# Kernel optimization log

Measured on AMD Instinct MI355X. Metric: run time of the kernel, lower is better.

Reference implementation:

```python
import jax, jax.numpy as jnp
import numpy as np

B, L, V = 2048, 200, 100000
EMB_DIM = 32      # emb_session_dim / emb_loc_dim (hardcoded 32 in __init__)
TIME_DIM = 128    # config['model']['timeemb']
LOC_DIM = 32
COND = TIME_DIM + LOC_DIM  # 160
NUM_STEPS = 50
MASK_TIME = 48    # pe[pos == 48] = 0 in the 2-D branch


def _time_embedding(pos, d_model):
    # sinusoidal embedding, interleaved sin/cos exactly as the torch code
    div = 1.0 / jnp.power(10000.0, jnp.arange(0, d_model, 2, dtype=jnp.float32) / d_model)
    ang = pos[..., None].astype(jnp.float32) * div           # [..., d_model//2]
    pe = jnp.zeros(pos.shape + (d_model,), jnp.float32)
    pe = pe.at[..., 0::2].set(jnp.sin(ang)).at[..., 1::2].set(jnp.cos(ang))
    return pe


def setup_inputs() -> dict:
    key = jax.random.key(0)
    ks = jax.random.split(key, 12)
    tp = jax.random.randint(ks[0], (B,), 0, 48, dtype=jnp.int32)
    loc = jax.random.randint(ks[1], (B,), 1, V + 1)            # 1-based loc ids
    emb = jax.random.normal(ks[2], (B, EMB_DIM), jnp.float32)
    s = jax.random.randint(ks[3], (B, L), 1, V + 1)
    tt = jax.random.randint(ks[4], (B, L), 0, 49)              # 48 == padding slot
    ST_traj = jnp.stack([s, tt], axis=-1)                      # [B, L, 2]
    loc_emb_all = jax.random.normal(ks[5], (V, LOC_DIM), jnp.float32) * 0.1
    noise = jax.random.normal(ks[6], (B, EMB_DIM), jnp.float32)
    t = jax.random.randint(ks[7], (B,), 0, NUM_STEPS)
    sc = COND ** -0.5
    w1 = jax.random.normal(ks[8], (COND, COND), jnp.float32) * sc
    w2 = jax.random.normal(ks[9], (COND, COND), jnp.float32) * sc
    b2 = jnp.zeros((COND,), jnp.float32)
    wc = jax.random.normal(ks[10], (COND,), jnp.float32) * sc
    beta = np.linspace(0.0001 ** 0.5, 0.5 ** 0.5, NUM_STEPS) ** 2  # 'quad' schedule
    alpha_hat = jnp.asarray(np.cumprod(1.0 - beta), jnp.float32)
    return {"tp": tp, "loc": loc, "emb": emb, "ST_traj": ST_traj,
            "loc_emb_all": loc_emb_all, "noise": noise, "t": t,
            "w1": w1, "w2": w2, "b2": b2, "wc": wc, "alpha_hat": alpha_hat}


def reference(tp, loc, emb, ST_traj, loc_emb_all, noise, t, w1, w2, b2, wc, alpha_hat):
    # --- diffusion noising (calc_loss prelude) ---
    a = alpha_hat[t][:, None]                                   # [B, 1]
    noisy = jnp.sqrt(a) * emb + jnp.sqrt(1.0 - a) * noise       # [B, EMB_DIM]

    # --- get_ST_info: sinusoid + single fused gather (replaces per-element index_select loop) ---
    te = _time_embedding(tp, TIME_DIM)                          # [B, TIME_DIM] (1-D branch: no mask)
    le = loc_emb_all[loc - 1]                                   # [B, LOC_DIM]
    side = jnp.concatenate([te, le], axis=-1)                   # [B, COND]
    ST_info = jnp.broadcast_to(side[:, :, None], (B, COND, EMB_DIM))

    # --- get_user_info: trajectory embed + soft_attn ---
    s = ST_traj[..., 0]
    ts = ST_traj[..., 1]
    te2 = _time_embedding(ts, TIME_DIM)                         # [B, L, TIME_DIM]
    te2 = jnp.where((ts == MASK_TIME)[..., None], 0.0, te2)     # pe[pos == 48] = 0
    le2 = loc_emb_all[s - 1]                                    # [B, L, LOC_DIM] fused gather
    ue = jnp.concatenate([le2, te2], axis=-1)                   # [B, L, COND]
    mean_e = jnp.mean(ue, axis=1, keepdims=True)                # [B, 1, COND]
    attn = jax.nn.sigmoid(mean_e @ w1.T + ue @ w2.T + b2)       # [B, L, COND]
    score = attn @ wc                                           # [B, L]  (weight_c)
    uemb = jnp.einsum('bl,bld->bd', score, ue)                  # [B, COND]
    user_info = jnp.broadcast_to(uemb[:, :, None], (B, COND, EMB_DIM))

    # pack: [B, 2*COND + 1, EMB_DIM]
    return jnp.concatenate([ST_info, user_info, noisy[:, None, :]], axis=1)
```

## Files before the change

kernel.cpp:

```cpp
#include <hip/hip_runtime.h>
#include <hip/hip_bf16.h>

#define LSEQ   200
#define LPAD   208
#define EMB    32
#define TDIM   128
#define COND   160
#define ROWS   321
#define MASK_T 48
#define LL_LDB 80

typedef __attribute__((ext_vector_type(8))) short          short8;
typedef __attribute__((ext_vector_type(4))) float          f32x4;

__device__ __forceinline__ float bf2f(unsigned short u) {
    union { unsigned int i; float f; } v; v.i = ((unsigned int)u) << 16; return v.f;
}
__device__ __forceinline__ float asf(unsigned int u) {
    union { unsigned int i; float f; } v; v.i = u; return v.f;
}
__device__ __forceinline__ unsigned int f2bf(float f) {
    union { float f; unsigned int i; } v; v.f = f;
    unsigned int x = v.i;
    return ((x + 0x7fffu + ((x >> 16) & 1u)) >> 16);
}
__device__ __forceinline__ unsigned int pack2(float lo, float hi) {
    return f2bf(lo) | (f2bf(hi) << 16);
}

template<int CTRL>
__device__ __forceinline__ float dpp_add(float v) {
    const int x = __builtin_amdgcn_update_dpp(0, __float_as_int(v), CTRL, 0xf, 0xf, true);
    return v + __int_as_float(x);
}
__device__ __forceinline__ float red16(float v) {
    v = dpp_add<0x128>(v);
    v = dpp_add<0x124>(v);
    v = dpp_add<0x122>(v);
    v = dpp_add<0x121>(v);
    return v;
}

__global__ void prep(const float* __restrict__ w1, const float* __restrict__ w2,
                     unsigned short* __restrict__ te_tab, float* __restrict__ T1t,
                     unsigned short* __restrict__ te_t, unsigned short* __restrict__ T2w3,
                     unsigned short* __restrict__ w2b) {
    __shared__ float te128[TDIM];
    const int t = blockIdx.x, tid = threadIdx.x;
    if (tid < 64) {
        const float dv = __expf(-0.14391156f * (float)tid);
        const float a  = (float)t * dv;
        const float s  = __sinf(a), c = __cosf(a);
        te128[2 * tid] = s; te128[2 * tid + 1] = c;
        ((unsigned int*)te_tab)[t * 64 + tid] = pack2(s, c);
    }
    __syncthreads();
    if (tid < COND) {
        float s1 = 0.0f, s2 = 0.0f;
        const float* w1r = w1 + tid * COND + EMB;
        const float* w2r = w2 + tid * COND + EMB;
        #pragma unroll 8
        for (int j = 0; j < TDIM; ++j) {
            s1 = fmaf(te128[j], w1r[j], s1);
            s2 = fmaf(te128[j], w2r[j], s2);
        }
        if (t == MASK_T) { s1 = 0.0f; s2 = 0.0f; }
        T1t[tid * 52 + t] = s1;
        const int tile = tid >> 4, lcc = tid & 15;
        T2w3[t * 256 + lcc * 16 + tile] = (unsigned short)f2bf(s2);
    }
    if (tid < TDIM) te_t[tid * 52 + t] = (unsigned short)f2bf(te128[tid]);
    if (t == 0 && tid < COND) {
        const float* src = w2 + (size_t)tid * COND;
        unsigned int* dst = (unsigned int*)(w2b + tid * 32);
        #pragma unroll
        for (int j = 0; j < 16; ++j)
            dst[j] = pack2(src[2 * j], src[2 * j + 1]);
    }
}

__global__ __launch_bounds__(256) __attribute__((amdgpu_waves_per_eu(4, 8)))
void fused4(const int*   __restrict__ tp,
            const int*   __restrict__ loc,
            const float* __restrict__ emb,
            const int*   __restrict__ st,
            const float* __restrict__ loc_emb,
            const float* __restrict__ noise,
            const int*   __restrict__ tstep,
            const float* __restrict__ w1,
            const unsigned short* __restrict__ w2b,
            const unsigned short* __restrict__ te_tab,
            const float* __restrict__ T1t,
            const unsigned short* __restrict__ te_t,
            const unsigned short* __restrict__ T2w3,
            const float* __restrict__ b2,
            const float* __restrict__ wc,
            const float* __restrict__ alpha_hat,
            float* __restrict__ out)
{
    __shared__ __attribute__((aligned(16))) unsigned char LL[LPAD * LL_LDB];
    __shared__ float scoreW[LSEQ];
    __shared__ float su[320];
    __shared__ float m1W[COND];
    __shared__ __attribute__((aligned(16))) float mupart[4][EMB];
    __shared__ __attribute__((aligned(16))) float cntsb[52];
    __shared__ __attribute__((aligned(4)))  unsigned char ttr[LPAD];

    const int tid  = threadIdx.x;
    const int w    = tid >> 6, lane = tid & 63;
    const int b    = blockIdx.x;
    const int lc   = lane & 15, lg = lane >> 4;
    const int rsub = lane >> 3, csub = lane & 7;
    const int2* st2 = (const int2*)st;
    float* outb = out + (size_t)b * (ROWS * EMB);

    short8 bf[10]; float wcv[10];
    #pragma unroll
    for (int T = 0; T < 10; ++T) {
        const int c = T * 16 + lc;
        bf[T]  = *(const short8*)(w2b + c * 32 + lg * 8);
        wcv[T] = wc[c];
    }

    if (w == 0) {
        if (lane < 32) {
            const ushort4 tv = *(const ushort4*)(te_tab + tp[b] * TDIM + lane * 4);
            f32x4 s4 = { bf2f(tv.x), bf2f(tv.y), bf2f(tv.z), bf2f(tv.w) };
            *(f32x4*)(su + lane * 4) = s4;
        } else if (lane < 40) {
            *(f32x4*)(su + 128 + (lane - 32) * 4) =
                *(const f32x4*)(loc_emb + (size_t)(loc[b] - 1) * EMB + (lane - 32) * 4);
        } else if (lane < 48) {
            const int e4 = lane - 40;
            const float a  = alpha_hat[tstep[b]];
            const float sa = sqrtf(a), sn = sqrtf(1.0f - a);
            const f32x4 ev = *(const f32x4*)(emb + (size_t)b * EMB + e4 * 4);
            const f32x4 nv = *(const f32x4*)(noise + (size_t)b * EMB + e4 * 4);
            f32x4 r = { sa*ev[0]+sn*nv[0], sa*ev[1]+sn*nv[1],
                        sa*ev[2]+sn*nv[2], sa*ev[3]+sn*nv[3] };
            *(f32x4*)(outb + 320 * EMB + e4 * 4) = r;
        }
    } else if (w == 1) {
        if (lane < 52) cntsb[lane] = 0.0f;
        if (lane >= 52 && lane < 60) {
            const int r = 200 + lane - 52;
            uint4 z = make_uint4(0, 0, 0, 0);
            *(uint4*)(LL + r * LL_LDB)      = z;
            *(uint4*)(LL + r * LL_LDB + 16) = z;
            *(uint4*)(LL + r * LL_LDB + 32) = z;
            *(uint4*)(LL + r * LL_LDB + 48) = z;
            ttr[r] = 0;
        }
    }
    __syncthreads();

    int tA = MASK_T;
    if (lane < 50) {
        const int r = w * 50 + lane;
        const int2 sv = st2[(size_t)b * LSEQ + r];
        ttr[r] = (unsigned char)sv.y;
        tA = sv.y;
        if (sv.y != MASK_T) atomicAdd(&cntsb[sv.y], 1.0f);
    }

    f32x4 macc = {0.f, 0.f, 0.f, 0.f};
    #pragma unroll
    for (int i = 0; i < 7; ++i) {
        const int rr = i * 8 + rsub;
        if (rr < 50) {
            const int row = w * 50 + rr;
            const int s0 = st2[(size_t)b * LSEQ + row].x - 1;
            const f32x4 v = *(const f32x4*)(loc_emb + (size_t)s0 * EMB + csub * 4);
            macc += v;
            uint2 pv = make_uint2(pack2(v[0], v[1]), pack2(v[2], v[3]));
            *(uint2*)(LL + row * LL_LDB + csub * 8) = pv;
        }
    }
    #pragma unroll
    for (int sh = 8; sh < 64; sh <<= 1) {
        macc[0] += __shfl_xor(macc[0], sh);
        macc[1] += __shfl_xor(macc[1], sh);
        macc[2] += __shfl_xor(macc[2], sh);
        macc[3] += __shfl_xor(macc[3], sh);
    }
    if (rsub == 0) *(f32x4*)(&mupart[w][csub * 4]) = macc;
    __syncthreads();

    if (tid < COND) {
        const int c = tid;
        f32x4 mm[8];
        #pragma unroll
        for (int j = 0; j < 8; ++j)
            mm[j] = ((const f32x4*)mupart[0])[j] + ((const f32x4*)mupart[1])[j]
                  + ((const f32x4*)mupart[2])[j] + ((const f32x4*)mupart[3])[j];
        f32x4 d = {0.f, 0.f, 0.f, 0.f};
        const f32x4* w1r = (const f32x4*)(w1 + (size_t)c * COND);
        #pragma unroll
        for (int j = 0; j < 8; ++j) d += mm[j] * w1r[j];
        const f32x4* t1r = (const f32x4*)(T1t + c * 52);
        #pragma unroll
        for (int q = 0; q < 13; ++q)
            d += ((const f32x4*)cntsb)[q] * t1r[q];
        m1W[c] = b2[c] + (d[0] + d[1] + d[2] + d[3]) * 0.005f;
    }
    __syncthreads();

    if (w == 1 && lane < 52) cntsb[lane] = 0.0f;

    float m1v[10];
    #pragma unroll
    for (int T = 0; T < 10; ++T) m1v[T] = m1W[T * 16 + lc];

    const int ms   = (w == 0) ? 0 : 3 * w + 1;
    const int mcnt = (w == 0) ? 4 : 3;
    for (int mi = 0; mi < mcnt; ++mi) {
        const int m = ms + mi;
        const short8 av = *(const short8*)(LL + (m * 16 + lc) * LL_LDB + lg * 16);
        const uchar4 tq = *(const uchar4*)(ttr + m * 16 + lg * 4);
        float s4[4] = {0.f, 0.f, 0.f, 0.f};

        #pragma unroll
        for (int g = 0; g < 2; ++g) {
            f32x4 acc[5];
            #pragma unroll
            for (int T5 = 0; T5 < 5; ++T5) {
                f32x4 z = {0.f, 0.f, 0.f, 0.f};
                acc[T5] = __builtin_amdgcn_mfma_f32_16x16x32_bf16(av, bf[g * 5 + T5], z, 0, 0, 0);
            }
            #pragma unroll
            for (int r = 0; r < 4; ++r) {
                const int t = (r == 0) ? tq.x : (r == 1) ? tq.y : (r == 2) ? tq.z : tq.w;
                const unsigned short* t2p = T2w3 + t * 256 + lc * 16 + g * 5;
                const ushort4 qa = *(const ushort4*)(t2p);
                const unsigned short q4 = t2p[4];
                #pragma unroll
                for (int T5 = 0; T5 < 5; ++T5) {
                    const int T = g * 5 + T5;
                    const unsigned short t2u =
                        (T5 == 0) ? qa.x : (T5 == 1) ? qa.y :
                        (T5 == 2) ? qa.z : (T5 == 3) ? qa.w : q4;
                    const float x = acc[T5][r] + m1v[T] + bf2f(t2u);
                    s4[r] = fmaf(wcv[T], __builtin_amdgcn_rcpf(1.0f + __expf(-x)), s4[r]);
                }
            }
        }
        f32x4 srow;
        srow[0] = red16(s4[0]); srow[1] = red16(s4[1]);
        srow[2] = red16(s4[2]); srow[3] = red16(s4[3]);
        if (lc == 0) {
            #pragma unroll
            for (int r = 0; r < 4; ++r) {
                const int row = m * 16 + lg * 4 + r;
                if (row < LSEQ) scoreW[row] = srow[r];
            }
        }
    }
    __syncthreads();

    if (lane < 50) {
        const float sc = scoreW[w * 50 + lane];
        if (tA != MASK_T) atomicAdd(&cntsb[tA], sc);
    }
    f32x4 uacc = {0.f, 0.f, 0.f, 0.f};
    #pragma unroll
    for (int i = 0; i < 7; ++i) {
        const int rr = i * 8 + rsub;
        if (rr < 50) {
            const int row = w * 50 + rr;
            const float sc = scoreW[row];
            const uint2 pv = *(const uint2*)(LL + row * LL_LDB + csub * 8);
            uacc[0] = fmaf(sc, asf(pv.x << 16), uacc[0]);
            uacc[1] = fmaf(sc, asf(pv.x & 0xffff0000u), uacc[1]);
            uacc[2] = fmaf(sc, asf(pv.y << 16), uacc[2]);
            uacc[3] = fmaf(sc, asf(pv.y & 0xffff0000u), uacc[3]);
        }
    }
    #pragma unroll
    for (int sh = 8; sh < 64; sh <<= 1) {
        uacc[0] += __shfl_xor(uacc[0], sh);
        uacc[1] += __shfl_xor(uacc[1], sh);
        uacc[2] += __shfl_xor(uacc[2], sh);
        uacc[3] += __shfl_xor(uacc[3], sh);
    }
    if (rsub == 0) *(f32x4*)(&mupart[w][csub * 4]) = uacc;
    __syncthreads();

    if (tid < TDIM) {
        const int j = tid;
        const unsigned short* ter = te_t + j * 52;
        float s = 0.0f;
        #pragma unroll
        for (int q = 0; q < 13; ++q) {
            const f32x4 sq = ((const f32x4*)cntsb)[q];
            const ushort4 tv = *(const ushort4*)(ter + q * 4);
            s = fmaf(sq[0], bf2f(tv.x), s);
            s = fmaf(sq[1], bf2f(tv.y), s);
            s = fmaf(sq[2], bf2f(tv.z), s);
            s = fmaf(sq[3], bf2f(tv.w), s);
        }
        su[192 + j] = s;
    } else if (tid < TDIM + 32) {
        const int col = tid - TDIM;
        su[160 + col] = mupart[0][col] + mupart[1][col]
                      + mupart[2][col] + mupart[3][col];
    }
    __syncthreads();

    #pragma unroll
    for (int k = 0; k < 10; ++k) {
        const int idx = tid + k * 256;
        const int row = idx >> 3;
        const float v = su[row];
        f32x4 vv = {v, v, v, v};
        *(f32x4*)(outb + row * EMB + (idx & 7) * 4) = vv;
    }
}

extern "C" void kernel_launch(void* const* d_in, const int* in_sizes, int n_in,
                              void* d_out, int out_size, void* d_ws, size_t ws_size,
                              hipStream_t stream) {
    const int*   tp        = (const int*)  d_in[0];
    const int*   loc       = (const int*)  d_in[1];
    const float* emb       = (const float*)d_in[2];
    const int*   st        = (const int*)  d_in[3];
    const float* loc_emb   = (const float*)d_in[4];
    const float* noise     = (const float*)d_in[5];
    const int*   tstep     = (const int*)  d_in[6];
    const float* w1        = (const float*)d_in[7];
    const float* w2        = (const float*)d_in[8];
    const float* b2        = (const float*)d_in[9];
    const float* wc        = (const float*)d_in[10];
    const float* alpha_hat = (const float*)d_in[11];
    float* out = (float*)d_out;

    char* ws = (char*)d_ws;
    float*          T1t    = (float*)ws;
    unsigned short* te_tab = (unsigned short*)(ws + 33280);
    unsigned short* te_t   = (unsigned short*)(ws + 45824);
    unsigned short* T2w3   = (unsigned short*)(ws + 59136);
    unsigned short* w2b    = (unsigned short*)(ws + 84224);

    prep<<<49, 256, 0, stream>>>(w1, w2, te_tab, T1t, te_t, T2w3, w2b);

    const int nb = in_sizes[0];
    fused4<<<nb, 256, 0, stream>>>(tp, loc, emb, st, loc_emb, noise, tstep,
                                   w1, w2b, te_tab, T1t, te_t, T2w3,
                                   b2, wc, alpha_hat, out);
}
```

Before: 71.71 us.

## Split attention score work across waves by output-column tiles instead of rows

Each wave now owns a slice of the 10 output column tiles (3,3,2,2) and loops over all 13 row blocks, instead of owning a range of rows with all 10 column tiles. Per-wave register use for the w2 B-fragments, m1 and wc values drops from 10 tiles to at most 3. The T2 table is re-laid out so each wave's slots are contiguous. Partial scores are combined with LDS atomicAdd into a zero-initialised scoreW. The trade-off is that every wave now reloads all A fragments and adds LDS atomics, in exchange for lower register pressure and a more even load across waves.

```diff
diff --git a/kernel.cpp b/kernel.cpp
--- a/kernel.cpp
+++ b/kernel.cpp
@@ -43,7 +43,7 @@
 
 __global__ void prep(const float* __restrict__ w1, const float* __restrict__ w2,
                      unsigned short* __restrict__ te_tab, float* __restrict__ T1t,
-                     unsigned short* __restrict__ te_t, unsigned short* __restrict__ T2w3,
+                     unsigned short* __restrict__ te_t, unsigned short* __restrict__ T2w4,
                      unsigned short* __restrict__ w2b) {
     __shared__ float te128[TDIM];
     const int t = blockIdx.x, tid = threadIdx.x;
@@ -67,7 +67,9 @@
         if (t == MASK_T) { s1 = 0.0f; s2 = 0.0f; }
         T1t[tid * 52 + t] = s1;
         const int tile = tid >> 4, lcc = tid & 15;
-        T2w3[t * 256 + lcc * 16 + tile] = (unsigned short)f2bf(s2);
+        const int wg   = (tile < 3) ? 0 : (tile < 6) ? 1 : (tile < 8) ? 2 : 3;
+        const int slot = tile - ((wg == 0) ? 0 : (wg == 1) ? 3 : (wg == 2) ? 6 : 8);
+        T2w4[t * 256 + lcc * 16 + wg * 4 + slot] = (unsigned short)f2bf(s2);
     }
     if (tid < TDIM) te_t[tid * 52 + t] = (unsigned short)f2bf(te128[tid]);
     if (t == 0 && tid < COND) {
@@ -92,7 +94,7 @@
             const unsigned short* __restrict__ te_tab,
             const float* __restrict__ T1t,
             const unsigned short* __restrict__ te_t,
-            const unsigned short* __restrict__ T2w3,
+            const unsigned short* __restrict__ T2w4,
             const float* __restrict__ b2,
             const float* __restrict__ wc,
             const float* __restrict__ alpha_hat,
@@ -113,14 +115,6 @@
     const int rsub = lane >> 3, csub = lane & 7;
     const int2* st2 = (const int2*)st;
     float* outb = out + (size_t)b * (ROWS * EMB);
-
-    short8 bf[10]; float wcv[10];
-    #pragma unroll
-    for (int T = 0; T < 10; ++T) {
-        const int c = T * 16 + lc;
-        bf[T]  = *(const short8*)(w2b + c * 32 + lg * 8);
-        wcv[T] = wc[c];
-    }
 
     if (w == 0) {
         if (lane < 32) {
@@ -142,6 +136,10 @@
         }
     } else if (w == 1) {
         if (lane < 52) cntsb[lane] = 0.0f;
+        if (lane < 50) {
+            f32x4 z = {0.f, 0.f, 0.f, 0.f};
+            *(f32x4*)(scoreW + lane * 4) = z;
+        }
         if (lane >= 52 && lane < 60) {
             const int r = 200 + lane - 52;
             uint4 z = make_uint4(0, 0, 0, 0);
@@ -207,51 +205,48 @@
 
     if (w == 1 && lane < 52) cntsb[lane] = 0.0f;
 
-    float m1v[10];
-    #pragma unroll
-    for (int T = 0; T < 10; ++T) m1v[T] = m1W[T * 16 + lc];
-
-    const int ms   = (w == 0) ? 0 : 3 * w + 1;
-    const int mcnt = (w == 0) ? 4 : 3;
-    for (int mi = 0; mi < mcnt; ++mi) {
-        const int m = ms + mi;
+    const int  t0  = (w < 2) ? 3 * w : 6 + 2 * (w - 2);
+    const bool tn3 = (w < 2);
+    short8 bf0, bf1, bf2v = short8{0,0,0,0,0,0,0,0};
+    float m10, m11, m12 = 0.0f, wc0, wc1, wc2 = 0.0f;
+    {
+        const int c0 = t0 * 16 + lc, c1 = (t0 + 1) * 16 + lc;
+        bf0 = *(const short8*)(w2b + c0 * 32 + lg * 8);
+        bf1 = *(const short8*)(w2b + c1 * 32 + lg * 8);
+        m10 = m1W[c0]; wc0 = wc[c0];
+        m11 = m1W[c1]; wc1 = wc[c1];
+        if (tn3) {
+            const int c2 = (t0 + 2) * 16 + lc;
+            bf2v = *(const short8*)(w2b + c2 * 32 + lg * 8);
+            m12 = m1W[c2]; wc2 = wc[c2];
+        }
+    }
+
+    for (int m = 0; m < 13; ++m) {
         const short8 av = *(const short8*)(LL + (m * 16 + lc) * LL_LDB + lg * 16);
         const uchar4 tq = *(const uchar4*)(ttr + m * 16 + lg * 4);
-        float s4[4] = {0.f, 0.f, 0.f, 0.f};
-
-        #pragma unroll
-        for (int g = 0; g < 2; ++g) {
-            f32x4 acc[5];
-            #pragma unroll
-            for (int T5 = 0; T5 < 5; ++T5) {
-                f32x4 z = {0.f, 0.f, 0.f, 0.f};
-                acc[T5] = __builtin_amdgcn_mfma_f32_16x16x32_bf16(av, bf[g * 5 + T5], z, 0, 0, 0);
-            }
-            #pragma unroll
-            for (int r = 0; r < 4; ++r) {
-                const int t = (r == 0) ? tq.x : (r == 1) ? tq.y : (r == 2) ? tq.z : tq.w;
-                const unsigned short* t2p = T2w3 + t * 256 + lc * 16 + g * 5;
-                const ushort4 qa = *(const ushort4*)(t2p);
-                const unsigned short q4 = t2p[4];
-                #pragma unroll
-                for (int T5 = 0; T5 < 5; ++T5) {
-                    const int T = g * 5 + T5;
-                    const unsigned short t2u =
-                        (T5 == 0) ? qa.x : (T5 == 1) ? qa.y :
-                        (T5 == 2) ? qa.z : (T5 == 3) ? qa.w : q4;
-                    const float x = acc[T5][r] + m1v[T] + bf2f(t2u);
-                    s4[r] = fmaf(wcv[T], __builtin_amdgcn_rcpf(1.0f + __expf(-x)), s4[r]);
-                }
-            }
-        }
+        f32x4 z = {0.f, 0.f, 0.f, 0.f};
+        f32x4 a0 = __builtin_amdgcn_mfma_f32_16x16x32_bf16(av, bf0, z, 0, 0, 0);
+        f32x4 a1 = __builtin_amdgcn_mfma_f32_16x16x32_bf16(av, bf1, z, 0, 0, 0);
+        f32x4 a2 = z;
+        if (tn3) a2 = __builtin_amdgcn_mfma_f32_16x16x32_bf16(av, bf2v, z, 0, 0, 0);
+
         f32x4 srow;
-        srow[0] = red16(s4[0]); srow[1] = red16(s4[1]);
-        srow[2] = red16(s4[2]); srow[3] = red16(s4[3]);
+        #pragma unroll
+        for (int r = 0; r < 4; ++r) {
+            const int t = (r == 0) ? tq.x : (r == 1) ? tq.y : (r == 2) ? tq.z : tq.w;
+            const ushort4 q = *(const ushort4*)(T2w4 + t * 256 + lc * 16 + w * 4);
+            float s = wc0 * __builtin_amdgcn_rcpf(1.0f + __expf(-(a0[r] + m10 + bf2f(q.x))))
+                    + wc1 * __builtin_amdgcn_rcpf(1.0f + __expf(-(a1[r] + m11 + bf2f(q.y))));
+            if (tn3)
+                s += wc2 * __builtin_amdgcn_rcpf(1.0f + __expf(-(a2[r] + m12 + bf2f(q.z))));
+            srow[r] = red16(s);
+        }
         if (lc == 0) {
             #pragma unroll
             for (int r = 0; r < 4; ++r) {
                 const int row = m * 16 + lg * 4 + r;
-                if (row < LSEQ) scoreW[row] = srow[r];
+                if (row < LSEQ) atomicAdd(&scoreW[row], srow[r]);
             }
         }
     }
@@ -337,13 +332,13 @@
     float*          T1t    = (float*)ws;
     unsigned short* te_tab = (unsigned short*)(ws + 33280);
     unsigned short* te_t   = (unsigned short*)(ws + 45824);
-    unsigned short* T2w3   = (unsigned short*)(ws + 59136);
+    unsigned short* T2w4   = (unsigned short*)(ws + 59136);
     unsigned short* w2b    = (unsigned short*)(ws + 84224);
 
-    prep<<<49, 256, 0, stream>>>(w1, w2, te_tab, T1t, te_t, T2w3, w2b);
+    prep<<<49, 256, 0, stream>>>(w1, w2, te_tab, T1t, te_t, T2w4, w2b);
 
     const int nb = in_sizes[0];
     fused4<<<nb, 256, 0, stream>>>(tp, loc, emb, st, loc_emb, noise, tstep,
-                                   w1, w2b, te_tab, T1t, te_t, T2w3,
+                                   w1, w2b, te_tab, T1t, te_t, T2w4,
                                    b2, wc, alpha_hat, out);
 }
```

New measurement: 116.8 us. 1.63x slower.

## Run one batch row per single-wave block, replacing barriers with LDS waits

Applied to the files above, without the earlier changes.

The fused kernel now uses one 64-lane wavefront per batch row instead of four waves. This removes __syncthreads and leaves only lgkmcnt waits. The bf16 LDS staging of gathered location embeddings is dropped: rows are re-gathered from global memory (the mean pass, the MFMA A operand, and the weighted-sum pass) and indices are kept in LDS. The MFMA work is split into two column groups so each holds five B fragments, with the T2 table relaid out to match. This trades inter-wave sync and LDS footprint for less per-block parallelism and repeated global gathers that rely on cache hits.

```diff
diff --git a/kernel.cpp b/kernel.cpp
--- a/kernel.cpp
+++ b/kernel.cpp
@@ -8,16 +8,14 @@
 #define COND   160
 #define ROWS   321
 #define MASK_T 48
-#define LL_LDB 80
-
-typedef __attribute__((ext_vector_type(8))) short          short8;
-typedef __attribute__((ext_vector_type(4))) float          f32x4;
+
+typedef __attribute__((ext_vector_type(8))) short  short8;
+typedef __attribute__((ext_vector_type(4))) float  f32x4;
+
+#define WAIT_LGKM() asm volatile("s_waitcnt lgkmcnt(0)" ::: "memory")
 
 __device__ __forceinline__ float bf2f(unsigned short u) {
     union { unsigned int i; float f; } v; v.i = ((unsigned int)u) << 16; return v.f;
-}
-__device__ __forceinline__ float asf(unsigned int u) {
-    union { unsigned int i; float f; } v; v.i = u; return v.f;
 }
 __device__ __forceinline__ unsigned int f2bf(float f) {
     union { float f; unsigned int i; } v; v.f = f;
@@ -26,6 +24,12 @@
 }
 __device__ __forceinline__ unsigned int pack2(float lo, float hi) {
     return f2bf(lo) | (f2bf(hi) << 16);
+}
+__device__ __forceinline__ short8 pack8(f32x4 a, f32x4 b) {
+    union { short8 s; unsigned int u[4]; } r;
+    r.u[0] = pack2(a[0], a[1]); r.u[1] = pack2(a[2], a[3]);
+    r.u[2] = pack2(b[0], b[1]); r.u[3] = pack2(b[2], b[3]);
+    return r.s;
 }
 
 template<int CTRL>
@@ -43,7 +47,7 @@
 
 __global__ void prep(const float* __restrict__ w1, const float* __restrict__ w2,
                      unsigned short* __restrict__ te_tab, float* __restrict__ T1t,
-                     unsigned short* __restrict__ te_t, unsigned short* __restrict__ T2w3,
+                     unsigned short* __restrict__ te_t, unsigned short* __restrict__ T2w2,
                      unsigned short* __restrict__ w2b) {
     __shared__ float te128[TDIM];
     const int t = blockIdx.x, tid = threadIdx.x;
@@ -67,7 +71,8 @@
         if (t == MASK_T) { s1 = 0.0f; s2 = 0.0f; }
         T1t[tid * 52 + t] = s1;
         const int tile = tid >> 4, lcc = tid & 15;
-        T2w3[t * 256 + lcc * 16 + tile] = (unsigned short)f2bf(s2);
+        const int g = (tile >= 5) ? 1 : 0, slot = tile - 5 * g;
+        T2w2[t * 256 + g * 128 + lcc * 8 + slot] = (unsigned short)f2bf(s2);
     }
     if (tid < TDIM) te_t[tid * 52 + t] = (unsigned short)f2bf(te128[tid]);
     if (t == 0 && tid < COND) {
@@ -79,8 +84,8 @@
     }
 }
 
-__global__ __launch_bounds__(256) __attribute__((amdgpu_waves_per_eu(4, 8)))
-void fused4(const int*   __restrict__ tp,
+__global__ __launch_bounds__(64) __attribute__((amdgpu_waves_per_eu(4, 8)))
+void fusedw(const int*   __restrict__ tp,
             const int*   __restrict__ loc,
             const float* __restrict__ emb,
             const int*   __restrict__ st,
@@ -92,89 +97,66 @@
             const unsigned short* __restrict__ te_tab,
             const float* __restrict__ T1t,
             const unsigned short* __restrict__ te_t,
-            const unsigned short* __restrict__ T2w3,
+            const unsigned short* __restrict__ T2w2,
             const float* __restrict__ b2,
             const float* __restrict__ wc,
             const float* __restrict__ alpha_hat,
             float* __restrict__ out)
 {
-    __shared__ __attribute__((aligned(16))) unsigned char LL[LPAD * LL_LDB];
+    __shared__ int   ssr[LPAD];
     __shared__ float scoreW[LSEQ];
     __shared__ float su[320];
     __shared__ float m1W[COND];
-    __shared__ __attribute__((aligned(16))) float mupart[4][EMB];
-    __shared__ __attribute__((aligned(16))) float cntsb[52];
-    __shared__ __attribute__((aligned(4)))  unsigned char ttr[LPAD];
-
-    const int tid  = threadIdx.x;
-    const int w    = tid >> 6, lane = tid & 63;
+    __shared__ __attribute__((aligned(16))) float mloc[EMB];
+    __shared__ __attribute__((aligned(16))) float cntW[52];
+    __shared__ __attribute__((aligned(16))) float sbW[52];
+    __shared__ __attribute__((aligned(4))) unsigned char ttr[LPAD];
+
+    const int lane = threadIdx.x;
     const int b    = blockIdx.x;
     const int lc   = lane & 15, lg = lane >> 4;
     const int rsub = lane >> 3, csub = lane & 7;
     const int2* st2 = (const int2*)st;
     float* outb = out + (size_t)b * (ROWS * EMB);
 
-    short8 bf[10]; float wcv[10];
-    #pragma unroll
-    for (int T = 0; T < 10; ++T) {
-        const int c = T * 16 + lc;
-        bf[T]  = *(const short8*)(w2b + c * 32 + lg * 8);
-        wcv[T] = wc[c];
-    }
-
-    if (w == 0) {
-        if (lane < 32) {
-            const ushort4 tv = *(const ushort4*)(te_tab + tp[b] * TDIM + lane * 4);
-            f32x4 s4 = { bf2f(tv.x), bf2f(tv.y), bf2f(tv.z), bf2f(tv.w) };
-            *(f32x4*)(su + lane * 4) = s4;
-        } else if (lane < 40) {
-            *(f32x4*)(su + 128 + (lane - 32) * 4) =
-                *(const f32x4*)(loc_emb + (size_t)(loc[b] - 1) * EMB + (lane - 32) * 4);
-        } else if (lane < 48) {
-            const int e4 = lane - 40;
-            const float a  = alpha_hat[tstep[b]];
-            const float sa = sqrtf(a), sn = sqrtf(1.0f - a);
-            const f32x4 ev = *(const f32x4*)(emb + (size_t)b * EMB + e4 * 4);
-            const f32x4 nv = *(const f32x4*)(noise + (size_t)b * EMB + e4 * 4);
-            f32x4 r = { sa*ev[0]+sn*nv[0], sa*ev[1]+sn*nv[1],
-                        sa*ev[2]+sn*nv[2], sa*ev[3]+sn*nv[3] };
-            *(f32x4*)(outb + 320 * EMB + e4 * 4) = r;
-        }
-    } else if (w == 1) {
-        if (lane < 52) cntsb[lane] = 0.0f;
-        if (lane >= 52 && lane < 60) {
-            const int r = 200 + lane - 52;
-            uint4 z = make_uint4(0, 0, 0, 0);
-            *(uint4*)(LL + r * LL_LDB)      = z;
-            *(uint4*)(LL + r * LL_LDB + 16) = z;
-            *(uint4*)(LL + r * LL_LDB + 32) = z;
-            *(uint4*)(LL + r * LL_LDB + 48) = z;
-            ttr[r] = 0;
-        }
-    }
-    __syncthreads();
-
-    int tA = MASK_T;
-    if (lane < 50) {
-        const int r = w * 50 + lane;
-        const int2 sv = st2[(size_t)b * LSEQ + r];
-        ttr[r] = (unsigned char)sv.y;
-        tA = sv.y;
-        if (sv.y != MASK_T) atomicAdd(&cntsb[sv.y], 1.0f);
-    }
+    if (lane < 52) { cntW[lane] = 0.0f; sbW[lane] = 0.0f; }
+    if (lane < 32) {
+        const ushort4 tv = *(const ushort4*)(te_tab + tp[b] * TDIM + lane * 4);
+        f32x4 s4 = { bf2f(tv.x), bf2f(tv.y), bf2f(tv.z), bf2f(tv.w) };
+        *(f32x4*)(su + lane * 4) = s4;
+    } else if (lane < 40) {
+        *(f32x4*)(su + 128 + (lane - 32) * 4) =
+            *(const f32x4*)(loc_emb + (size_t)(loc[b] - 1) * EMB + (lane - 32) * 4);
+    } else if (lane < 48) {
+        const int e4 = lane - 40;
+        const float a  = alpha_hat[tstep[b]];
+        const float sa = sqrtf(a), sn = sqrtf(1.0f - a);
+        const f32x4 ev = *(const f32x4*)(emb + (size_t)b * EMB + e4 * 4);
+        const f32x4 nv = *(const f32x4*)(noise + (size_t)b * EMB + e4 * 4);
+        f32x4 r = { sa*ev[0]+sn*nv[0], sa*ev[1]+sn*nv[1],
+                    sa*ev[2]+sn*nv[2], sa*ev[3]+sn*nv[3] };
+        *(f32x4*)(outb + 320 * EMB + e4 * 4) = r;
+    }
+
+    #pragma unroll
+    for (int k = 0; k < 4; ++k) {
+        const int r = lane + k * 64;
+        if (r < LSEQ) {
+            const int2 sv = st2[(size_t)b * LSEQ + r];
+            ttr[r] = (unsigned char)sv.y;
+            ssr[r] = sv.x;
+            if (sv.y != MASK_T) atomicAdd(&cntW[sv.y], 1.0f);
+        } else if (r < LPAD) {
+            ttr[r] = 0; ssr[r] = 1;
+        }
+    }
+    WAIT_LGKM();
 
     f32x4 macc = {0.f, 0.f, 0.f, 0.f};
-    #pragma unroll
-    for (int i = 0; i < 7; ++i) {
-        const int rr = i * 8 + rsub;
-        if (rr < 50) {
-            const int row = w * 50 + rr;
-            const int s0 = st2[(size_t)b * LSEQ + row].x - 1;
-            const f32x4 v = *(const f32x4*)(loc_emb + (size_t)s0 * EMB + csub * 4);
-            macc += v;
-            uint2 pv = make_uint2(pack2(v[0], v[1]), pack2(v[2], v[3]));
-            *(uint2*)(LL + row * LL_LDB + csub * 8) = pv;
-        }
+    for (int i = 0; i < 25; ++i) {
+        const int row = rsub * 25 + i;
+        const int s0 = ssr[row] - 1;
+        macc += *(const f32x4*)(loc_emb + (size_t)s0 * EMB + csub * 4);
     }
     #pragma unroll
     for (int sh = 8; sh < 64; sh <<= 1) {
@@ -183,97 +165,103 @@
         macc[2] += __shfl_xor(macc[2], sh);
         macc[3] += __shfl_xor(macc[3], sh);
     }
-    if (rsub == 0) *(f32x4*)(&mupart[w][csub * 4]) = macc;
-    __syncthreads();
-
-    if (tid < COND) {
-        const int c = tid;
+    if (rsub == 0) *(f32x4*)(mloc + csub * 4) = macc;
+    WAIT_LGKM();
+
+    {
         f32x4 mm[8];
         #pragma unroll
-        for (int j = 0; j < 8; ++j)
-            mm[j] = ((const f32x4*)mupart[0])[j] + ((const f32x4*)mupart[1])[j]
-                  + ((const f32x4*)mupart[2])[j] + ((const f32x4*)mupart[3])[j];
-        f32x4 d = {0.f, 0.f, 0.f, 0.f};
-        const f32x4* w1r = (const f32x4*)(w1 + (size_t)c * COND);
-        #pragma unroll
-        for (int j = 0; j < 8; ++j) d += mm[j] * w1r[j];
-        const f32x4* t1r = (const f32x4*)(T1t + c * 52);
-        #pragma unroll
-        for (int q = 0; q < 13; ++q)
-            d += ((const f32x4*)cntsb)[q] * t1r[q];
-        m1W[c] = b2[c] + (d[0] + d[1] + d[2] + d[3]) * 0.005f;
-    }
-    __syncthreads();
-
-    if (w == 1 && lane < 52) cntsb[lane] = 0.0f;
-
-    float m1v[10];
-    #pragma unroll
-    for (int T = 0; T < 10; ++T) m1v[T] = m1W[T * 16 + lc];
-
-    const int ms   = (w == 0) ? 0 : 3 * w + 1;
-    const int mcnt = (w == 0) ? 4 : 3;
-    for (int mi = 0; mi < mcnt; ++mi) {
-        const int m = ms + mi;
-        const short8 av = *(const short8*)(LL + (m * 16 + lc) * LL_LDB + lg * 16);
-        const uchar4 tq = *(const uchar4*)(ttr + m * 16 + lg * 4);
-        float s4[4] = {0.f, 0.f, 0.f, 0.f};
-
-        #pragma unroll
-        for (int g = 0; g < 2; ++g) {
+        for (int j = 0; j < 8; ++j) mm[j] = ((const f32x4*)mloc)[j];
+        #pragma unroll
+        for (int k = 0; k < 3; ++k) {
+            const int c = lane + k * 64;
+            if (c < COND) {
+                f32x4 d = {0.f, 0.f, 0.f, 0.f};
+                const f32x4* w1r = (const f32x4*)(w1 + (size_t)c * COND);
+                #pragma unroll
+                for (int j = 0; j < 8; ++j) d += mm[j] * w1r[j];
+                const f32x4* t1r = (const f32x4*)(T1t + c * 52);
+                #pragma unroll
+                for (int q = 0; q < 13; ++q)
+                    d += ((const f32x4*)cntW)[q] * t1r[q];
+                m1W[c] = b2[c] + (d[0] + d[1] + d[2] + d[3]) * 0.005f;
+            }
+        }
+    }
+    WAIT_LGKM();
+
+    #pragma unroll 1
+    for (int g = 0; g < 2; ++g) {
+        short8 bf[5]; float m1v[5], wcv[5];
+        #pragma unroll
+        for (int T5 = 0; T5 < 5; ++T5) {
+            const int c = (g * 5 + T5) * 16 + lc;
+            bf[T5]  = *(const short8*)(w2b + c * 32 + lg * 8);
+            m1v[T5] = m1W[c];
+            wcv[T5] = wc[c];
+        }
+        for (int m = 0; m < 13; ++m) {
+            const int sA = ssr[m * 16 + lc] - 1;
+            const uchar4 tq = *(const uchar4*)(ttr + m * 16 + lg * 4);
+            const f32x4* ar = (const f32x4*)(loc_emb + (size_t)sA * EMB + lg * 8);
+            const short8 av = pack8(ar[0], ar[1]);
+
             f32x4 acc[5];
             #pragma unroll
             for (int T5 = 0; T5 < 5; ++T5) {
                 f32x4 z = {0.f, 0.f, 0.f, 0.f};
-                acc[T5] = __builtin_amdgcn_mfma_f32_16x16x32_bf16(av, bf[g * 5 + T5], z, 0, 0, 0);
+                acc[T5] = __builtin_amdgcn_mfma_f32_16x16x32_bf16(av, bf[T5], z, 0, 0, 0);
             }
+            f32x4 srow;
             #pragma unroll
             for (int r = 0; r < 4; ++r) {
                 const int t = (r == 0) ? tq.x : (r == 1) ? tq.y : (r == 2) ? tq.z : tq.w;
-                const unsigned short* t2p = T2w3 + t * 256 + lc * 16 + g * 5;
+                const unsigned short* t2p = T2w2 + t * 256 + g * 128 + lc * 8;
                 const ushort4 qa = *(const ushort4*)(t2p);
                 const unsigned short q4 = t2p[4];
+                float s = 0.0f;
                 #pragma unroll
                 for (int T5 = 0; T5 < 5; ++T5) {
-                    const int T = g * 5 + T5;
                     const unsigned short t2u =
                         (T5 == 0) ? qa.x : (T5 == 1) ? qa.y :
                         (T5 == 2) ? qa.z : (T5 == 3) ? qa.w : q4;
-                    const float x = acc[T5][r] + m1v[T] + bf2f(t2u);
-                    s4[r] = fmaf(wcv[T], __builtin_amdgcn_rcpf(1.0f + __expf(-x)), s4[r]);
+                    const float x = acc[T5][r] + m1v[T5] + bf2f(t2u);
+                    s = fmaf(wcv[T5], __builtin_amdgcn_rcpf(1.0f + __expf(-x)), s);
+                }
+                srow[r] = red16(s);
+            }
+            if (lc == 0) {
+                #pragma unroll
+                for (int r = 0; r < 4; ++r) {
+                    const int row = m * 16 + lg * 4 + r;
+                    if (row < LSEQ) {
+                        if (g == 0) scoreW[row] = srow[r];
+                        else        scoreW[row] += srow[r];
+                    }
                 }
             }
         }
-        f32x4 srow;
-        srow[0] = red16(s4[0]); srow[1] = red16(s4[1]);
-        srow[2] = red16(s4[2]); srow[3] = red16(s4[3]);
-        if (lc == 0) {
-            #pragma unroll
-            for (int r = 0; r < 4; ++r) {
-                const int row = m * 16 + lg * 4 + r;
-                if (row < LSEQ) scoreW[row] = srow[r];
-            }
-        }
-    }
-    __syncthreads();
-
-    if (lane < 50) {
-        const float sc = scoreW[w * 50 + lane];
-        if (tA != MASK_T) atomicAdd(&cntsb[tA], sc);
+        WAIT_LGKM();
+    }
+
+    #pragma unroll
+    for (int k = 0; k < 4; ++k) {
+        const int r = lane + k * 64;
+        if (r < LSEQ) {
+            const int tt = ttr[r];
+            if (tt != MASK_T) atomicAdd(&sbW[tt], scoreW[r]);
+        }
     }
     f32x4 uacc = {0.f, 0.f, 0.f, 0.f};
-    #pragma unroll
-    for (int i = 0; i < 7; ++i) {
-        const int rr = i * 8 + rsub;
-        if (rr < 50) {
-            const int row = w * 50 + rr;
-            const float sc = scoreW[row];
-            const uint2 pv = *(const uint2*)(LL + row * LL_LDB + csub * 8);
-            uacc[0] = fmaf(sc, asf(pv.x << 16), uacc[0]);
-            uacc[1] = fmaf(sc, asf(pv.x & 0xffff0000u), uacc[1]);
-            uacc[2] = fmaf(sc, asf(pv.y << 16), uacc[2]);
-            uacc[3] = fmaf(sc, asf(pv.y & 0xffff0000u), uacc[3]);
-        }
+    for (int i = 0; i < 25; ++i) {
+        const int row = rsub * 25 + i;
+        const int s0 = ssr[row] - 1;
+        const float sc = scoreW[row];
+        const f32x4 v = *(const f32x4*)(loc_emb + (size_t)s0 * EMB + csub * 4);
+        uacc[0] = fmaf(sc, v[0], uacc[0]);
+        uacc[1] = fmaf(sc, v[1], uacc[1]);
+        uacc[2] = fmaf(sc, v[2], uacc[2]);
+        uacc[3] = fmaf(sc, v[3], uacc[3]);
     }
     #pragma unroll
     for (int sh = 8; sh < 64; sh <<= 1) {
@@ -282,16 +270,17 @@
         uacc[2] += __shfl_xor(uacc[2], sh);
         uacc[3] += __shfl_xor(uacc[3], sh);
     }
-    if (rsub == 0) *(f32x4*)(&mupart[w][csub * 4]) = uacc;
-    __syncthreads();
-
-    if (tid < TDIM) {
-        const int j = tid;
+    if (rsub == 0) *(f32x4*)(su + 160 + csub * 4) = uacc;
+    WAIT_LGKM();
+
+    #pragma unroll
+    for (int k = 0; k < 2; ++k) {
+        const int j = lane + k * 64;
         const unsigned short* ter = te_t + j * 52;
         float s = 0.0f;
         #pragma unroll
         for (int q = 0; q < 13; ++q) {
-            const f32x4 sq = ((const f32x4*)cntsb)[q];
+            const f32x4 sq = ((const f32x4*)sbW)[q];
             const ushort4 tv = *(const ushort4*)(ter + q * 4);
             s = fmaf(sq[0], bf2f(tv.x), s);
             s = fmaf(sq[1], bf2f(tv.y), s);
@@ -299,16 +288,12 @@
             s = fmaf(sq[3], bf2f(tv.w), s);
         }
         su[192 + j] = s;
-    } else if (tid < TDIM + 32) {
-        const int col = tid - TDIM;
-        su[160 + col] = mupart[0][col] + mupart[1][col]
-                      + mupart[2][col] + mupart[3][col];
-    }
-    __syncthreads();
-
-    #pragma unroll
-    for (int k = 0; k < 10; ++k) {
-        const int idx = tid + k * 256;
+    }
+    WAIT_LGKM();
+
+    #pragma unroll 4
+    for (int k = 0; k < 40; ++k) {
+        const int idx = lane + k * 64;
         const int row = idx >> 3;
         const float v = su[row];
         f32x4 vv = {v, v, v, v};
@@ -337,13 +322,13 @@
     float*          T1t    = (float*)ws;
     unsigned short* te_tab = (unsigned short*)(ws + 33280);
     unsigned short* te_t   = (unsigned short*)(ws + 45824);
-    unsigned short* T2w3   = (unsigned short*)(ws + 59136);
+    unsigned short* T2w2   = (unsigned short*)(ws + 59136);
     unsigned short* w2b    = (unsigned short*)(ws + 84224);
 
-    prep<<<49, 256, 0, stream>>>(w1, w2, te_tab, T1t, te_t, T2w3, w2b);
+    prep<<<49, 256, 0, stream>>>(w1, w2, te_tab, T1t, te_t, T2w2, w2b);
 
     const int nb = in_sizes[0];
-    fused4<<<nb, 256, 0, stream>>>(tp, loc, emb, st, loc_emb, noise, tstep,
-                                   w1, w2b, te_tab, T1t, te_t, T2w3,
-                                   b2, wc, alpha_hat, out);
-}
+    fusedw<<<nb, 64, 0, stream>>>(tp, loc, emb, st, loc_emb, noise, tstep,
+                                  w1, w2b, te_tab, T1t, te_t, T2w2,
+                                  b2, wc, alpha_hat, out);
+}
```

Measured after the change: 85.78 us. +19.6%, slower.
